# Kernel tuning notes

Measured on AMD Instinct MI355X. Metric: run time of the kernel, lower is better.

Reference implementation:

```python
import jax, jax.numpy as jnp
import numpy as np
import math

B, S, D, H = 2, 2048, 768, 12
HD = D // H


def setup_inputs() -> dict:
    key = jax.random.key(0)
    ks = jax.random.split(key, 9)
    scale = 1.0 / math.sqrt(D)
    x = jax.random.normal(ks[0], (B, S, D), dtype=jnp.float32)
    # causal mask: True where attention is allowed (query i attends to key j<=i)
    mask = jnp.tril(jnp.ones((S, S), dtype=bool))[None, None]  # [1,1,S,S]
    wq = jax.random.normal(ks[1], (D, D), dtype=jnp.float32) * scale
    bq = jnp.zeros((D,), dtype=jnp.float32)
    wk = jax.random.normal(ks[2], (D, D), dtype=jnp.float32) * scale
    bk = jnp.zeros((D,), dtype=jnp.float32)
    wv = jax.random.normal(ks[3], (D, D), dtype=jnp.float32) * scale
    bv = jnp.zeros((D,), dtype=jnp.float32)
    wo = jax.random.normal(ks[4], (D, D), dtype=jnp.float32) * scale
    bo = jnp.zeros((D,), dtype=jnp.float32)
    return {"x": x, "mask": mask, "wq": wq, "bq": bq, "wk": wk, "bk": bk,
            "wv": wv, "bv": bv, "wo": wo, "bo": bo}


def reference(x, mask, wq, bq, wk, bk, wv, bv, wo, bo):
    b, s, d = x.shape
    # projections (flax Linear: y = x @ kernel + bias)
    q = (x @ wq + bq).reshape(b, s, H, HD).transpose(0, 2, 1, 3)  # [b,h,s,hd]
    k = (x @ wk + bk).reshape(b, s, H, HD).transpose(0, 2, 1, 3)
    v = (x @ wv + bv).reshape(b, s, H, HD).transpose(0, 2, 1, 3)
    scores = jnp.einsum('bhqd,bhkd->bhqk', q, k) / math.sqrt(HD)  # [b,h,s,s]
    scores = jnp.where(mask, scores, -jnp.inf)
    attn = jax.nn.softmax(scores, axis=-1)
    out = jnp.einsum('bhqk,bhkd->bhqd', attn, v)  # [b,h,s,hd]
    out = out.transpose(0, 2, 1, 3).reshape(b, s, d)
    return out @ wo + bo
```

## Files before the change

kernel.cpp:

```cpp
#include <hip/hip_runtime.h>
#include <math.h>

#define BATCH 2
#define SEQ   2048
#define DMODEL 768
#define NHEAD 12
#define HDIM  64

typedef unsigned short u16;
typedef __attribute__((ext_vector_type(8))) short bf16x8;
typedef __attribute__((ext_vector_type(4))) float f32x4;
typedef __attribute__((ext_vector_type(8))) unsigned short us8;
typedef __attribute__((ext_vector_type(4))) unsigned short us4;

__device__ __forceinline__ u16 f2bf(float f) {
    union { float f; unsigned u; } v; v.f = f;
    unsigned u = v.u;
    u += 0x7fff + ((u >> 16) & 1);
    return (u16)(u >> 16);
}

__device__ __forceinline__ u16 f2bf_trunc(float f) {
    union { float f; unsigned u; } v; v.f = f;
    return (u16)(v.u >> 16);
}

__device__ __forceinline__ void g2l16(const void* g, void* l) {
    __builtin_amdgcn_global_load_lds(
        (const __attribute__((address_space(1))) unsigned int*)g,
        (__attribute__((address_space(3))) unsigned int*)(unsigned int)(unsigned long long)(uintptr_t)l,
        16, 0, 0);
}

__global__ __launch_bounds__(256) void prep(const float* __restrict__ x,
                                            const float* __restrict__ w0,
                                            const float* __restrict__ w1,
                                            const float* __restrict__ w2,
                                            const float* __restrict__ w3,
                                            u16* __restrict__ xb,
                                            u16* __restrict__ Wt_all) {
    __shared__ float t[32][33];
    const int bid = blockIdx.x;
    if (bid < 3072) {
        int i = bid * 256 + threadIdx.x;
        float4 v = ((const float4*)x)[i];
        us4 o;
        o.x = f2bf(v.x); o.y = f2bf(v.y); o.z = f2bf(v.z); o.w = f2bf(v.w);
        *(us4*)&xb[(size_t)i * 4] = o;
    } else {
        const int wid = bid - 3072;
        const int z  = wid / 576;
        const int rr = wid % 576;
        const int by = rr / 24, bx = rr % 24;
        const float* W = z == 0 ? w0 : z == 1 ? w1 : z == 2 ? w2 : w3;
        u16* Wt = Wt_all + (size_t)z * DMODEL * DMODEL;

        int tx = threadIdx.x & 31, ty = threadIdx.x >> 5;
        int xg = bx * 32 + tx;
        #pragma unroll
        for (int j = 0; j < 32; j += 8)
            t[ty + j][tx] = W[(size_t)(by * 32 + ty + j) * DMODEL + xg];
        __syncthreads();
        int x2 = by * 32 + tx;
        #pragma unroll
        for (int j = 0; j < 32; j += 8)
            Wt[(size_t)(bx * 32 + ty + j) * DMODEL + x2] = f2bf(t[tx][ty + j]);
    }
}

__device__ __forceinline__ void mfma_loop(const u16* __restrict__ Ag,
                                          const u16* __restrict__ Bt,
                                          int m0, int n0, int tid,
                                          u16* As, u16* Bs,
                                          f32x4 acc[4][4]) {
    const int lane = tid & 63;
    const int quad = lane >> 4, l16 = lane & 15;
    const int w    = tid >> 6;
    const int wm   = w >> 1, wn = w & 1;
    const int rowA = tid >> 2;
    const int kch  = (tid & 3) * 8;

    for (int k0 = 0; k0 < DMODEL; k0 += 32) {
        const u16* Agk = Ag + (size_t)m0 * DMODEL + k0;
        const u16* Btk = Bt + (size_t)n0 * DMODEL + k0;
        g2l16(Agk + (size_t)rowA * DMODEL + kch,        As + tid * 8);
        g2l16(Agk + (size_t)(rowA + 64) * DMODEL + kch, As + 2048 + tid * 8);
        g2l16(Btk + (size_t)rowA * DMODEL + kch,        Bs + tid * 8);
        g2l16(Btk + (size_t)(rowA + 64) * DMODEL + kch, Bs + 2048 + tid * 8);
        __syncthreads();

        bf16x8 af[4], bfr[4];
        #pragma unroll
        for (int i = 0; i < 4; ++i)
            af[i] = *(const bf16x8*)&As[(wm * 64 + i * 16 + l16) * 32 + quad * 8];
        #pragma unroll
        for (int j = 0; j < 4; ++j)
            bfr[j] = *(const bf16x8*)&Bs[(wn * 64 + j * 16 + l16) * 32 + quad * 8];
        #pragma unroll
        for (int i = 0; i < 4; ++i)
            #pragma unroll
            for (int j = 0; j < 4; ++j)
                acc[i][j] = __builtin_amdgcn_mfma_f32_16x16x32_bf16(af[i], bfr[j], acc[i][j], 0, 0, 0);
        __syncthreads();
    }
}

__global__ __launch_bounds__(256) void gemm_qkv(
    const u16* __restrict__ xb, const u16* __restrict__ WtQK,
    const u16* __restrict__ WtV,
    const float* __restrict__ bq, const float* __restrict__ bk,
    const float* __restrict__ bv,
    u16* __restrict__ QK, u16* __restrict__ Vt) {

    __shared__ __align__(16) u16 As[128 * 32];
    __shared__ __align__(16) u16 Bs[128 * 32];

    const int tid  = threadIdx.x;
    const int lane = tid & 63;
    const int w    = tid >> 6;
    const int quad = lane >> 4, l16 = lane & 15;
    const int wm   = w >> 1, wn = w & 1;
    const int bid  = blockIdx.x;

    f32x4 acc[4][4] = {};

    if (bid < 384) {
        const int m0 = (bid & 31) * 128, n0 = (bid >> 5) * 128;
        mfma_loop(xb, WtQK, m0, n0, tid, As, Bs, acc);

        const size_t n_elem = (size_t)BATCH * SEQ * DMODEL;
        #pragma unroll
        for (int j = 0; j < 4; ++j) {
            const int n     = n0 + wn * 64 + j * 16 + l16;
            const int which = n / 768;
            const int nn    = n - which * 768;
            const float bias  = (which == 0 ? bq : bk)[nn];
            const float scale = (which == 0) ? 0.125f : 1.0f;
            const int h = nn >> 6, hd = nn & 63;
            u16* outw = QK + (size_t)which * n_elem;
            #pragma unroll
            for (int i = 0; i < 4; ++i) {
                const int mbase = m0 + wm * 64 + i * 16 + quad * 4;
                #pragma unroll
                for (int r = 0; r < 4; ++r) {
                    const int m  = mbase + r;
                    const int b_ = m >> 11, s_ = m & 2047;
                    outw[(size_t)((b_ * NHEAD + h) * SEQ + s_) * HDIM + hd] =
                        f2bf((acc[i][j][r] + bias) * scale);
                }
            }
        }
    } else {
        const int vid = bid - 384;
        const int m0 = (vid % 6) * 128, n0 = (vid / 6) * 128;
        mfma_loop(WtV, xb, m0, n0, tid, As, Bs, acc);

        #pragma unroll
        for (int i = 0; i < 4; ++i) {
            const int rbase = m0 + wm * 64 + i * 16 + quad * 4;
            #pragma unroll
            for (int r = 0; r < 4; ++r) {
                const int row_g = rbase + r;
                const float bias = bv[row_g];
                const int h = row_g >> 6, hd = row_g & 63;
                #pragma unroll
                for (int j = 0; j < 4; ++j) {
                    const int col_g = n0 + wn * 64 + j * 16 + l16;
                    const int b_ = col_g >> 11, s_ = col_g & 2047;
                    Vt[(size_t)((b_ * NHEAD + h) * HDIM + hd) * SEQ + s_] =
                        f2bf(acc[i][j][r] + bias);
                }
            }
        }
    }
}

__global__ __launch_bounds__(256) void gemm_out(
    const u16* __restrict__ Ag, const u16* __restrict__ Bt,
    const float* __restrict__ bo, float* __restrict__ out) {

    __shared__ __align__(16) u16 As[64 * 32];
    __shared__ __align__(16) u16 Bs[64 * 32];

    const int tid  = threadIdx.x;
    const int lane = tid & 63;
    const int w    = tid >> 6;
    const int quad = lane >> 4, l16 = lane & 15;
    const int wm   = w >> 1, wn = w & 1;
    const int m0 = blockIdx.x * 64, n0 = blockIdx.y * 64;

    const int rowA = tid >> 2;
    const int kch  = (tid & 3) * 8;

    f32x4 acc[2][2] = {};

    for (int k0 = 0; k0 < DMODEL; k0 += 32) {
        g2l16(Ag + (size_t)(m0 + rowA) * DMODEL + k0 + kch, As + tid * 8);
        g2l16(Bt + (size_t)(n0 + rowA) * DMODEL + k0 + kch, Bs + tid * 8);
        __syncthreads();

        bf16x8 af[2], bfr[2];
        #pragma unroll
        for (int i = 0; i < 2; ++i)
            af[i] = *(const bf16x8*)&As[(wm * 32 + i * 16 + l16) * 32 + quad * 8];
        #pragma unroll
        for (int j = 0; j < 2; ++j)
            bfr[j] = *(const bf16x8*)&Bs[(wn * 32 + j * 16 + l16) * 32 + quad * 8];
        #pragma unroll
        for (int i = 0; i < 2; ++i)
            #pragma unroll
            for (int j = 0; j < 2; ++j)
                acc[i][j] = __builtin_amdgcn_mfma_f32_16x16x32_bf16(af[i], bfr[j], acc[i][j], 0, 0, 0);
        __syncthreads();
    }

    #pragma unroll
    for (int i = 0; i < 2; ++i) {
        const int mbase = m0 + wm * 32 + i * 16 + quad * 4;
        #pragma unroll
        for (int r = 0; r < 4; ++r) {
            const int m = mbase + r;
            #pragma unroll
            for (int j = 0; j < 2; ++j) {
                const int n = n0 + wn * 32 + j * 16 + l16;
                out[(size_t)m * DMODEL + n] = acc[i][j][r] + bo[n];
            }
        }
    }
}

__global__ __launch_bounds__(256) void flash_attn_mfma(
    const u16* __restrict__ Q, const u16* __restrict__ K,
    const u16* __restrict__ Vt, u16* __restrict__ A) {

    __shared__ __align__(16) u16 Kl[64 * 72];
    __shared__ __align__(16) u16 Vl[64 * 72];
    __shared__ __align__(16) u16 Pl[4][16 * 72];

    const int tid  = threadIdx.x;
    const int lane = tid & 63;
    const int w    = tid >> 6;
    const int quad = lane >> 4;
    const int l16  = lane & 15;

    const int bh = blockIdx.x;
    const int p  = blockIdx.y;
    const int uq = (w < 2) ? p : 63 - p;
    const int wrow0 = uq * 32 + (w & 1) * 16;
    const int wlast = wrow0 + 15;

    const size_t base = (size_t)bh * SEQ * HDIM;
    const u16* Qg = Q + base;
    const u16* Kg = K + base;
    const u16* Vg = Vt + base;

    bf16x8 qf0 = *(const bf16x8*)&Qg[(size_t)(wrow0 + l16) * 64 + quad * 8];
    bf16x8 qf1 = *(const bf16x8*)&Qg[(size_t)(wrow0 + l16) * 64 + quad * 8 + 32];

    f32x4 o[4] = {};
    float l_acc[4] = {0.f, 0.f, 0.f, 0.f};

    const int qrow = wrow0 + quad * 4;
    const int uB = 63 - p;
    const int tc = (32 * uB + 31) / 64 + 1;

    for (int t2 = 0; t2 < tc; ++t2) {
        const int j0 = t2 * 64;
        __syncthreads();

        #pragma unroll
        for (int r = 0; r < 2; ++r) {
            int e = tid + r * 256;
            int row = e >> 3, col = (e & 7) * 8;
            *(us8*)&Kl[row * 72 + col] = *(const us8*)&Kg[(size_t)(j0 + row) * 64 + col];
        }
        #pragma unroll
        for (int r = 0; r < 2; ++r) {
            int e = tid + r * 256;
            int d = e >> 3, kc = (e & 7) * 8;
            *(us8*)&Vl[d * 72 + kc] = *(const us8*)&Vg[(size_t)d * SEQ + j0 + kc];
        }
        __syncthreads();

        if (j0 > wlast) continue;

        f32x4 s[4];
        #pragma unroll
        for (int c4 = 0; c4 < 4; ++c4) {
            bf16x8 kf0 = *(const bf16x8*)&Kl[(c4 * 16 + l16) * 72 + quad * 8];
            bf16x8 kf1 = *(const bf16x8*)&Kl[(c4 * 16 + l16) * 72 + quad * 8 + 32];
            f32x4 a2 = {};
            a2 = __builtin_amdgcn_mfma_f32_16x16x32_bf16(qf0, kf0, a2, 0, 0, 0);
            a2 = __builtin_amdgcn_mfma_f32_16x16x32_bf16(qf1, kf1, a2, 0, 0, 0);
            s[c4] = a2;
        }

        if (j0 + 63 > wrow0) {
            #pragma unroll
            for (int c4 = 0; c4 < 4; ++c4) {
                int jg = j0 + c4 * 16 + l16;
                #pragma unroll
                for (int r = 0; r < 4; ++r)
                    if (jg > qrow + r) s[c4][r] = -INFINITY;
            }
        }

        #pragma unroll
        for (int c4 = 0; c4 < 4; ++c4)
            #pragma unroll
            for (int r = 0; r < 4; ++r)
                s[c4][r] = __expf(s[c4][r]);
        #pragma unroll
        for (int r = 0; r < 4; ++r)
            l_acc[r] += (s[0][r] + s[1][r]) + (s[2][r] + s[3][r]);

        u16* Pw = Pl[w];
        #pragma unroll
        for (int c4 = 0; c4 < 4; ++c4)
            #pragma unroll
            for (int r = 0; r < 4; ++r)
                Pw[(quad * 4 + r) * 72 + c4 * 16 + l16] = f2bf_trunc(s[c4][r]);
        bf16x8 pf0 = *(const bf16x8*)&Pw[l16 * 72 + quad * 8];
        bf16x8 pf1 = *(const bf16x8*)&Pw[l16 * 72 + quad * 8 + 32];

        #pragma unroll
        for (int c2 = 0; c2 < 4; ++c2) {
            bf16x8 vf0 = *(const bf16x8*)&Vl[(c2 * 16 + l16) * 72 + quad * 8];
            bf16x8 vf1 = *(const bf16x8*)&Vl[(c2 * 16 + l16) * 72 + quad * 8 + 32];
            o[c2] = __builtin_amdgcn_mfma_f32_16x16x32_bf16(pf0, vf0, o[c2], 0, 0, 0);
            o[c2] = __builtin_amdgcn_mfma_f32_16x16x32_bf16(pf1, vf1, o[c2], 0, 0, 0);
        }
    }

    #pragma unroll
    for (int off = 1; off < 16; off <<= 1)
        #pragma unroll
        for (int r = 0; r < 4; ++r)
            l_acc[r] += __shfl_xor(l_acc[r], off);

    const int b = bh / NHEAD, h = bh % NHEAD;
    #pragma unroll
    for (int r = 0; r < 4; ++r) {
        float inv = 1.0f / l_acc[r];
        int sg = qrow + r;
        u16* dst = A + ((size_t)(b * SEQ + sg)) * DMODEL + h * HDIM;
        #pragma unroll
        for (int c2 = 0; c2 < 4; ++c2)
            dst[c2 * 16 + l16] = f2bf(o[c2][r] * inv);
    }
}

extern "C" void kernel_launch(void* const* d_in, const int* in_sizes, int n_in,
                              void* d_out, int out_size, void* d_ws, size_t ws_size,
                              hipStream_t stream) {
    const float* x  = (const float*)d_in[0];
    const float* wq = (const float*)d_in[2];
    const float* bq = (const float*)d_in[3];
    const float* wk = (const float*)d_in[4];
    const float* bk = (const float*)d_in[5];
    const float* wv = (const float*)d_in[6];
    const float* bv = (const float*)d_in[7];
    const float* wo = (const float*)d_in[8];
    const float* bo = (const float*)d_in[9];
    float* out = (float*)d_out;

    const size_t n_elem = (size_t)BATCH * SEQ * DMODEL;
    const size_t w_elem = (size_t)DMODEL * DMODEL;

    u16* xb     = (u16*)d_ws;
    u16* Wt_all = xb + n_elem;
    u16* Qw     = Wt_all + 4 * w_elem;
    u16* Kw     = Qw + n_elem;
    u16* Vtw    = Kw + n_elem;
    u16* Aw     = Vtw + n_elem;

    dim3 blk(256);

    prep<<<dim3(3072 + 2304), blk, 0, stream>>>(x, wq, wk, wv, wo, xb, Wt_all);

    gemm_qkv<<<dim3(384 + 192), blk, 0, stream>>>(xb, Wt_all,
                                                  Wt_all + 2 * w_elem,
                                                  bq, bk, bv, Qw, Vtw);

    flash_attn_mfma<<<dim3(24, 32), blk, 0, stream>>>(Qw, Kw, Vtw, Aw);

    gemm_out<<<dim3(64, 12), blk, 0, stream>>>(Aw, Wt_all + 3 * w_elem, bo, out);
}
```

Baseline: 180.7 us.

## Fuse all four kernels into one persistent kernel with grid barriers

Replaces the four separate launches (prep, QKV GEMM, flash attention, output GEMM) with a single 768-block kernel whose stages are separated by atomic-counter grid barriers. The QKV GEMM tiles are reshaped to 128x96 and 96x128 so every block has work in each stage. The aim is to remove launch gaps and tail effects between kernels. The cost is barrier spin overhead, an extra memset launch, and the assumption that all 768 blocks are co-resident, which risks deadlock otherwise.

Result: slower. 540.9 us (+199.3%).

```diff
diff --git a/kernel.cpp b/kernel.cpp
--- a/kernel.cpp
+++ b/kernel.cpp
@@ -6,6 +6,7 @@
 #define DMODEL 768
 #define NHEAD 12
 #define HDIM  64
+#define NBLK  768
 
 typedef unsigned short u16;
 typedef __attribute__((ext_vector_type(8))) short bf16x8;
@@ -32,112 +33,124 @@
         16, 0, 0);
 }
 
-__global__ __launch_bounds__(256) void prep(const float* __restrict__ x,
-                                            const float* __restrict__ w0,
-                                            const float* __restrict__ w1,
-                                            const float* __restrict__ w2,
-                                            const float* __restrict__ w3,
-                                            u16* __restrict__ xb,
-                                            u16* __restrict__ Wt_all) {
-    __shared__ float t[32][33];
-    const int bid = blockIdx.x;
-    if (bid < 3072) {
-        int i = bid * 256 + threadIdx.x;
-        float4 v = ((const float4*)x)[i];
-        us4 o;
-        o.x = f2bf(v.x); o.y = f2bf(v.y); o.z = f2bf(v.z); o.w = f2bf(v.w);
-        *(us4*)&xb[(size_t)i * 4] = o;
-    } else {
-        const int wid = bid - 3072;
-        const int z  = wid / 576;
-        const int rr = wid % 576;
-        const int by = rr / 24, bx = rr % 24;
-        const float* W = z == 0 ? w0 : z == 1 ? w1 : z == 2 ? w2 : w3;
-        u16* Wt = Wt_all + (size_t)z * DMODEL * DMODEL;
-
-        int tx = threadIdx.x & 31, ty = threadIdx.x >> 5;
-        int xg = bx * 32 + tx;
-        #pragma unroll
-        for (int j = 0; j < 32; j += 8)
-            t[ty + j][tx] = W[(size_t)(by * 32 + ty + j) * DMODEL + xg];
-        __syncthreads();
-        int x2 = by * 32 + tx;
-        #pragma unroll
-        for (int j = 0; j < 32; j += 8)
-            Wt[(size_t)(bx * 32 + ty + j) * DMODEL + x2] = f2bf(t[tx][ty + j]);
-    }
-}
-
-__device__ __forceinline__ void mfma_loop(const u16* __restrict__ Ag,
-                                          const u16* __restrict__ Bt,
-                                          int m0, int n0, int tid,
-                                          u16* As, u16* Bs,
-                                          f32x4 acc[4][4]) {
-    const int lane = tid & 63;
-    const int quad = lane >> 4, l16 = lane & 15;
-    const int w    = tid >> 6;
-    const int wm   = w >> 1, wn = w & 1;
-    const int rowA = tid >> 2;
-    const int kch  = (tid & 3) * 8;
-
-    for (int k0 = 0; k0 < DMODEL; k0 += 32) {
-        const u16* Agk = Ag + (size_t)m0 * DMODEL + k0;
-        const u16* Btk = Bt + (size_t)n0 * DMODEL + k0;
-        g2l16(Agk + (size_t)rowA * DMODEL + kch,        As + tid * 8);
-        g2l16(Agk + (size_t)(rowA + 64) * DMODEL + kch, As + 2048 + tid * 8);
-        g2l16(Btk + (size_t)rowA * DMODEL + kch,        Bs + tid * 8);
-        g2l16(Btk + (size_t)(rowA + 64) * DMODEL + kch, Bs + 2048 + tid * 8);
-        __syncthreads();
-
-        bf16x8 af[4], bfr[4];
-        #pragma unroll
-        for (int i = 0; i < 4; ++i)
-            af[i] = *(const bf16x8*)&As[(wm * 64 + i * 16 + l16) * 32 + quad * 8];
-        #pragma unroll
-        for (int j = 0; j < 4; ++j)
-            bfr[j] = *(const bf16x8*)&Bs[(wn * 64 + j * 16 + l16) * 32 + quad * 8];
-        #pragma unroll
-        for (int i = 0; i < 4; ++i)
-            #pragma unroll
-            for (int j = 0; j < 4; ++j)
-                acc[i][j] = __builtin_amdgcn_mfma_f32_16x16x32_bf16(af[i], bfr[j], acc[i][j], 0, 0, 0);
-        __syncthreads();
-    }
-}
-
-__global__ __launch_bounds__(256) void gemm_qkv(
-    const u16* __restrict__ xb, const u16* __restrict__ WtQK,
-    const u16* __restrict__ WtV,
+__device__ __forceinline__ void grid_barrier(unsigned* cnt, unsigned target) {
+    __syncthreads();
+    if (threadIdx.x == 0) {
+        __threadfence();
+        atomicAdd(cnt, 1u);
+        while (__hip_atomic_load(cnt, __ATOMIC_RELAXED,
+                                 __HIP_MEMORY_SCOPE_AGENT) < target)
+            __builtin_amdgcn_s_sleep(8);
+        __threadfence();
+    }
+    __syncthreads();
+}
+
+__device__ __forceinline__ void stage_rows(const u16* g, u16* lds, int nrows,
+                                           int tid) {
+    const int row = tid >> 2, col = (tid & 3) * 8;
+    g2l16(g + (size_t)row * DMODEL + col, lds + tid * 8);
+    if (nrows == 128) {
+        g2l16(g + (size_t)(row + 64) * DMODEL + col, lds + 2048 + tid * 8);
+    } else if (nrows == 96) {
+        if (tid < 128)
+            g2l16(g + (size_t)(row + 64) * DMODEL + col, lds + 2048 + tid * 8);
+    }
+}
+
+__global__ __launch_bounds__(256, 4) void fused(
+    const float* __restrict__ x,
+    const float* __restrict__ w0, const float* __restrict__ w1,
+    const float* __restrict__ w2, const float* __restrict__ w3,
     const float* __restrict__ bq, const float* __restrict__ bk,
-    const float* __restrict__ bv,
-    u16* __restrict__ QK, u16* __restrict__ Vt) {
-
-    __shared__ __align__(16) u16 As[128 * 32];
-    __shared__ __align__(16) u16 Bs[128 * 32];
-
+    const float* __restrict__ bv, const float* __restrict__ bo,
+    u16* xb, u16* Wt_all, u16* Qw, u16* Vtw, u16* Aw,
+    float* out, unsigned* cnt) {
+
+    __shared__ union {
+        struct { u16 A[128 * 32]; u16 B[128 * 32]; } g;
+        struct { u16 Kl[64 * 72]; u16 Vl[64 * 72];
+                 u16 Pl[4][16 * 72]; } f;
+        float t[32][33];
+    } sm;
+
+    const int b    = blockIdx.x;
     const int tid  = threadIdx.x;
     const int lane = tid & 63;
     const int w    = tid >> 6;
     const int quad = lane >> 4, l16 = lane & 15;
     const int wm   = w >> 1, wn = w & 1;
-    const int bid  = blockIdx.x;
-
-    f32x4 acc[4][4] = {};
-
-    if (bid < 384) {
-        const int m0 = (bid & 31) * 128, n0 = (bid >> 5) * 128;
-        mfma_loop(xb, WtQK, m0, n0, tid, As, Bs, acc);
-
-        const size_t n_elem = (size_t)BATCH * SEQ * DMODEL;
-        #pragma unroll
-        for (int j = 0; j < 4; ++j) {
-            const int n     = n0 + wn * 64 + j * 16 + l16;
+
+    const size_t n_elem = (size_t)BATCH * SEQ * DMODEL;
+    const size_t w_elem = (size_t)DMODEL * DMODEL;
+    const u16* WtQK = Wt_all;
+    const u16* WtV  = Wt_all + 2 * w_elem;
+    const u16* WtO  = Wt_all + 3 * w_elem;
+    u16* Kw = Qw + n_elem;
+
+    #pragma unroll 1
+    for (int ui = 0; ui < 7; ++ui) {
+        const int u = b * 7 + ui;
+        if (u < 3072) {
+            int i = u * 256 + tid;
+            float4 v = ((const float4*)x)[i];
+            us4 o;
+            o.x = f2bf(v.x); o.y = f2bf(v.y); o.z = f2bf(v.z); o.w = f2bf(v.w);
+            *(us4*)&xb[(size_t)i * 4] = o;
+        } else {
+            const int wid = u - 3072;
+            const int z  = wid / 576;
+            const int rr = wid % 576;
+            const int by = rr / 24, bx = rr % 24;
+            const float* W = z == 0 ? w0 : z == 1 ? w1 : z == 2 ? w2 : w3;
+            u16* Wt = Wt_all + (size_t)z * w_elem;
+            int tx = tid & 31, ty = tid >> 5;
+            int xg = bx * 32 + tx;
+            #pragma unroll
+            for (int j = 0; j < 32; j += 8)
+                sm.t[ty + j][tx] = W[(size_t)(by * 32 + ty + j) * DMODEL + xg];
+            __syncthreads();
+            int x2 = by * 32 + tx;
+            #pragma unroll
+            for (int j = 0; j < 32; j += 8)
+                Wt[(size_t)(bx * 32 + ty + j) * DMODEL + x2] = f2bf(sm.t[tx][ty + j]);
+            __syncthreads();
+        }
+    }
+
+    grid_barrier(cnt, NBLK);
+
+    if (b < 512) {
+        const int m0 = (b >> 4) * 128;
+        const int n0 = (b & 15) * 96;
+        f32x4 acc[4][3] = {};
+        for (int k0 = 0; k0 < DMODEL; k0 += 32) {
+            stage_rows(xb  + (size_t)m0 * DMODEL + k0, sm.g.A, 128, tid);
+            stage_rows(WtQK + (size_t)n0 * DMODEL + k0, sm.g.B,  96, tid);
+            __syncthreads();
+            bf16x8 af[4], bfr[3];
+            #pragma unroll
+            for (int i = 0; i < 4; ++i)
+                af[i] = *(const bf16x8*)&sm.g.A[(wm * 64 + i * 16 + l16) * 32 + quad * 8];
+            #pragma unroll
+            for (int j = 0; j < 3; ++j)
+                bfr[j] = *(const bf16x8*)&sm.g.B[(wn * 48 + j * 16 + l16) * 32 + quad * 8];
+            #pragma unroll
+            for (int i = 0; i < 4; ++i)
+                #pragma unroll
+                for (int j = 0; j < 3; ++j)
+                    acc[i][j] = __builtin_amdgcn_mfma_f32_16x16x32_bf16(af[i], bfr[j], acc[i][j], 0, 0, 0);
+            __syncthreads();
+        }
+        #pragma unroll
+        for (int j = 0; j < 3; ++j) {
+            const int n     = n0 + wn * 48 + j * 16 + l16;
             const int which = n / 768;
             const int nn    = n - which * 768;
             const float bias  = (which == 0 ? bq : bk)[nn];
             const float scale = (which == 0) ? 0.125f : 1.0f;
             const int h = nn >> 6, hd = nn & 63;
-            u16* outw = QK + (size_t)which * n_elem;
+            u16* outw = Qw + (size_t)which * n_elem;
             #pragma unroll
             for (int i = 0; i < 4; ++i) {
                 const int mbase = m0 + wm * 64 + i * 16 + quad * 4;
@@ -151,13 +164,31 @@
             }
         }
     } else {
-        const int vid = bid - 384;
-        const int m0 = (vid % 6) * 128, n0 = (vid / 6) * 128;
-        mfma_loop(WtV, xb, m0, n0, tid, As, Bs, acc);
-
-        #pragma unroll
-        for (int i = 0; i < 4; ++i) {
-            const int rbase = m0 + wm * 64 + i * 16 + quad * 4;
+        const int vj = b - 512;
+        const int m0 = (vj & 7) * 96;
+        const int n0 = (vj >> 3) * 128;
+        f32x4 acc[3][4] = {};
+        for (int k0 = 0; k0 < DMODEL; k0 += 32) {
+            stage_rows(WtV + (size_t)m0 * DMODEL + k0, sm.g.A,  96, tid);
+            stage_rows(xb  + (size_t)n0 * DMODEL + k0, sm.g.B, 128, tid);
+            __syncthreads();
+            bf16x8 af[3], bfr[4];
+            #pragma unroll
+            for (int i = 0; i < 3; ++i)
+                af[i] = *(const bf16x8*)&sm.g.A[(wm * 48 + i * 16 + l16) * 32 + quad * 8];
+            #pragma unroll
+            for (int j = 0; j < 4; ++j)
+                bfr[j] = *(const bf16x8*)&sm.g.B[(wn * 64 + j * 16 + l16) * 32 + quad * 8];
+            #pragma unroll
+            for (int i = 0; i < 3; ++i)
+                #pragma unroll
+                for (int j = 0; j < 4; ++j)
+                    acc[i][j] = __builtin_amdgcn_mfma_f32_16x16x32_bf16(af[i], bfr[j], acc[i][j], 0, 0, 0);
+            __syncthreads();
+        }
+        #pragma unroll
+        for (int i = 0; i < 3; ++i) {
+            const int rbase = m0 + wm * 48 + i * 16 + quad * 4;
             #pragma unroll
             for (int r = 0; r < 4; ++r) {
                 const int row_g = rbase + r;
@@ -167,186 +198,161 @@
                 for (int j = 0; j < 4; ++j) {
                     const int col_g = n0 + wn * 64 + j * 16 + l16;
                     const int b_ = col_g >> 11, s_ = col_g & 2047;
-                    Vt[(size_t)((b_ * NHEAD + h) * HDIM + hd) * SEQ + s_] =
+                    Vtw[(size_t)((b_ * NHEAD + h) * HDIM + hd) * SEQ + s_] =
                         f2bf(acc[i][j][r] + bias);
                 }
             }
         }
     }
-}
-
-__global__ __launch_bounds__(256) void gemm_out(
-    const u16* __restrict__ Ag, const u16* __restrict__ Bt,
-    const float* __restrict__ bo, float* __restrict__ out) {
-
-    __shared__ __align__(16) u16 As[64 * 32];
-    __shared__ __align__(16) u16 Bs[64 * 32];
-
-    const int tid  = threadIdx.x;
-    const int lane = tid & 63;
-    const int w    = tid >> 6;
-    const int quad = lane >> 4, l16 = lane & 15;
-    const int wm   = w >> 1, wn = w & 1;
-    const int m0 = blockIdx.x * 64, n0 = blockIdx.y * 64;
-
-    const int rowA = tid >> 2;
-    const int kch  = (tid & 3) * 8;
-
-    f32x4 acc[2][2] = {};
-
-    for (int k0 = 0; k0 < DMODEL; k0 += 32) {
-        g2l16(Ag + (size_t)(m0 + rowA) * DMODEL + k0 + kch, As + tid * 8);
-        g2l16(Bt + (size_t)(n0 + rowA) * DMODEL + k0 + kch, Bs + tid * 8);
-        __syncthreads();
-
-        bf16x8 af[2], bfr[2];
-        #pragma unroll
-        for (int i = 0; i < 2; ++i)
-            af[i] = *(const bf16x8*)&As[(wm * 32 + i * 16 + l16) * 32 + quad * 8];
-        #pragma unroll
-        for (int j = 0; j < 2; ++j)
-            bfr[j] = *(const bf16x8*)&Bs[(wn * 32 + j * 16 + l16) * 32 + quad * 8];
-        #pragma unroll
-        for (int i = 0; i < 2; ++i)
+
+    grid_barrier(cnt, 2 * NBLK);
+
+    {
+        const int bh = b % 24;
+        const int p  = b / 24;
+        const int uq = (w < 2) ? p : 63 - p;
+        const int wrow0 = uq * 32 + (w & 1) * 16;
+        const int wlast = wrow0 + 15;
+
+        const size_t base = (size_t)bh * SEQ * HDIM;
+        const u16* Qg = Qw + base;
+        const u16* Kg = Kw + base;
+        const u16* Vg = Vtw + base;
+
+        bf16x8 qf0 = *(const bf16x8*)&Qg[(size_t)(wrow0 + l16) * 64 + quad * 8];
+        bf16x8 qf1 = *(const bf16x8*)&Qg[(size_t)(wrow0 + l16) * 64 + quad * 8 + 32];
+
+        f32x4 o[4] = {};
+        float l_acc[4] = {0.f, 0.f, 0.f, 0.f};
+
+        const int qrow = wrow0 + quad * 4;
+        const int uB = 63 - p;
+        const int tc = (32 * uB + 31) / 64 + 1;
+
+        for (int t2 = 0; t2 < tc; ++t2) {
+            const int j0 = t2 * 64;
+            __syncthreads();
+            #pragma unroll
+            for (int r = 0; r < 2; ++r) {
+                int e = tid + r * 256;
+                int row = e >> 3, col = (e & 7) * 8;
+                *(us8*)&sm.f.Kl[row * 72 + col] =
+                    *(const us8*)&Kg[(size_t)(j0 + row) * 64 + col];
+            }
+            #pragma unroll
+            for (int r = 0; r < 2; ++r) {
+                int e = tid + r * 256;
+                int d = e >> 3, kc = (e & 7) * 8;
+                *(us8*)&sm.f.Vl[d * 72 + kc] =
+                    *(const us8*)&Vg[(size_t)d * SEQ + j0 + kc];
+            }
+            __syncthreads();
+
+            if (j0 > wlast) continue;
+
+            f32x4 s[4];
+            #pragma unroll
+            for (int c4 = 0; c4 < 4; ++c4) {
+                bf16x8 kf0 = *(const bf16x8*)&sm.f.Kl[(c4 * 16 + l16) * 72 + quad * 8];
+                bf16x8 kf1 = *(const bf16x8*)&sm.f.Kl[(c4 * 16 + l16) * 72 + quad * 8 + 32];
+                f32x4 a2 = {};
+                a2 = __builtin_amdgcn_mfma_f32_16x16x32_bf16(qf0, kf0, a2, 0, 0, 0);
+                a2 = __builtin_amdgcn_mfma_f32_16x16x32_bf16(qf1, kf1, a2, 0, 0, 0);
+                s[c4] = a2;
+            }
+
+            if (j0 + 63 > wrow0) {
+                #pragma unroll
+                for (int c4 = 0; c4 < 4; ++c4) {
+                    int jg = j0 + c4 * 16 + l16;
+                    #pragma unroll
+                    for (int r = 0; r < 4; ++r)
+                        if (jg > qrow + r) s[c4][r] = -INFINITY;
+                }
+            }
+
+            #pragma unroll
+            for (int c4 = 0; c4 < 4; ++c4)
+                #pragma unroll
+                for (int r = 0; r < 4; ++r)
+                    s[c4][r] = __expf(s[c4][r]);
+            #pragma unroll
+            for (int r = 0; r < 4; ++r)
+                l_acc[r] += (s[0][r] + s[1][r]) + (s[2][r] + s[3][r]);
+
+            u16* Pw = sm.f.Pl[w];
+            #pragma unroll
+            for (int c4 = 0; c4 < 4; ++c4)
+                #pragma unroll
+                for (int r = 0; r < 4; ++r)
+                    Pw[(quad * 4 + r) * 72 + c4 * 16 + l16] = f2bf_trunc(s[c4][r]);
+            bf16x8 pf0 = *(const bf16x8*)&Pw[l16 * 72 + quad * 8];
+            bf16x8 pf1 = *(const bf16x8*)&Pw[l16 * 72 + quad * 8 + 32];
+
+            #pragma unroll
+            for (int c2 = 0; c2 < 4; ++c2) {
+                bf16x8 vf0 = *(const bf16x8*)&sm.f.Vl[(c2 * 16 + l16) * 72 + quad * 8];
+                bf16x8 vf1 = *(const bf16x8*)&sm.f.Vl[(c2 * 16 + l16) * 72 + quad * 8 + 32];
+                o[c2] = __builtin_amdgcn_mfma_f32_16x16x32_bf16(pf0, vf0, o[c2], 0, 0, 0);
+                o[c2] = __builtin_amdgcn_mfma_f32_16x16x32_bf16(pf1, vf1, o[c2], 0, 0, 0);
+            }
+        }
+
+        #pragma unroll
+        for (int off = 1; off < 16; off <<= 1)
+            #pragma unroll
+            for (int r = 0; r < 4; ++r)
+                l_acc[r] += __shfl_xor(l_acc[r], off);
+
+        const int bb = bh / NHEAD, h = bh % NHEAD;
+        #pragma unroll
+        for (int r = 0; r < 4; ++r) {
+            float inv = 1.0f / l_acc[r];
+            int sg = qrow + r;
+            u16* dst = Aw + ((size_t)(bb * SEQ + sg)) * DMODEL + h * HDIM;
+            #pragma unroll
+            for (int c2 = 0; c2 < 4; ++c2)
+                dst[c2 * 16 + l16] = f2bf(o[c2][r] * inv);
+        }
+    }
+
+    grid_barrier(cnt, 3 * NBLK);
+
+    {
+        const int m0 = (b & 63) * 64;
+        const int n0 = (b >> 6) * 64;
+        f32x4 acc[2][2] = {};
+        for (int k0 = 0; k0 < DMODEL; k0 += 32) {
+            stage_rows(Aw  + (size_t)m0 * DMODEL + k0, sm.g.A, 64, tid);
+            stage_rows(WtO + (size_t)n0 * DMODEL + k0, sm.g.B, 64, tid);
+            __syncthreads();
+            bf16x8 af[2], bfr[2];
+            #pragma unroll
+            for (int i = 0; i < 2; ++i)
+                af[i] = *(const bf16x8*)&sm.g.A[(wm * 32 + i * 16 + l16) * 32 + quad * 8];
             #pragma unroll
             for (int j = 0; j < 2; ++j)
-                acc[i][j] = __builtin_amdgcn_mfma_f32_16x16x32_bf16(af[i], bfr[j], acc[i][j], 0, 0, 0);
-        __syncthreads();
-    }
-
-    #pragma unroll
-    for (int i = 0; i < 2; ++i) {
-        const int mbase = m0 + wm * 32 + i * 16 + quad * 4;
-        #pragma unroll
-        for (int r = 0; r < 4; ++r) {
-            const int m = mbase + r;
-            #pragma unroll
-            for (int j = 0; j < 2; ++j) {
-                const int n = n0 + wn * 32 + j * 16 + l16;
-                out[(size_t)m * DMODEL + n] = acc[i][j][r] + bo[n];
-            }
-        }
-    }
-}
-
-__global__ __launch_bounds__(256) void flash_attn_mfma(
-    const u16* __restrict__ Q, const u16* __restrict__ K,
-    const u16* __restrict__ Vt, u16* __restrict__ A) {
-
-    __shared__ __align__(16) u16 Kl[64 * 72];
-    __shared__ __align__(16) u16 Vl[64 * 72];
-    __shared__ __align__(16) u16 Pl[4][16 * 72];
-
-    const int tid  = threadIdx.x;
-    const int lane = tid & 63;
-    const int w    = tid >> 6;
-    const int quad = lane >> 4;
-    const int l16  = lane & 15;
-
-    const int bh = blockIdx.x;
-    const int p  = blockIdx.y;
-    const int uq = (w < 2) ? p : 63 - p;
-    const int wrow0 = uq * 32 + (w & 1) * 16;
-    const int wlast = wrow0 + 15;
-
-    const size_t base = (size_t)bh * SEQ * HDIM;
-    const u16* Qg = Q + base;
-    const u16* Kg = K + base;
-    const u16* Vg = Vt + base;
-
-    bf16x8 qf0 = *(const bf16x8*)&Qg[(size_t)(wrow0 + l16) * 64 + quad * 8];
-    bf16x8 qf1 = *(const bf16x8*)&Qg[(size_t)(wrow0 + l16) * 64 + quad * 8 + 32];
-
-    f32x4 o[4] = {};
-    float l_acc[4] = {0.f, 0.f, 0.f, 0.f};
-
-    const int qrow = wrow0 + quad * 4;
-    const int uB = 63 - p;
-    const int tc = (32 * uB + 31) / 64 + 1;
-
-    for (int t2 = 0; t2 < tc; ++t2) {
-        const int j0 = t2 * 64;
-        __syncthreads();
-
-        #pragma unroll
-        for (int r = 0; r < 2; ++r) {
-            int e = tid + r * 256;
-            int row = e >> 3, col = (e & 7) * 8;
-            *(us8*)&Kl[row * 72 + col] = *(const us8*)&Kg[(size_t)(j0 + row) * 64 + col];
-        }
-        #pragma unroll
-        for (int r = 0; r < 2; ++r) {
-            int e = tid + r * 256;
-            int d = e >> 3, kc = (e & 7) * 8;
-            *(us8*)&Vl[d * 72 + kc] = *(const us8*)&Vg[(size_t)d * SEQ + j0 + kc];
-        }
-        __syncthreads();
-
-        if (j0 > wlast) continue;
-
-        f32x4 s[4];
-        #pragma unroll
-        for (int c4 = 0; c4 < 4; ++c4) {
-            bf16x8 kf0 = *(const bf16x8*)&Kl[(c4 * 16 + l16) * 72 + quad * 8];
-            bf16x8 kf1 = *(const bf16x8*)&Kl[(c4 * 16 + l16) * 72 + quad * 8 + 32];
-            f32x4 a2 = {};
-            a2 = __builtin_amdgcn_mfma_f32_16x16x32_bf16(qf0, kf0, a2, 0, 0, 0);
-            a2 = __builtin_amdgcn_mfma_f32_16x16x32_bf16(qf1, kf1, a2, 0, 0, 0);
-            s[c4] = a2;
-        }
-
-        if (j0 + 63 > wrow0) {
-            #pragma unroll
-            for (int c4 = 0; c4 < 4; ++c4) {
-                int jg = j0 + c4 * 16 + l16;
-                #pragma unroll
-                for (int r = 0; r < 4; ++r)
-                    if (jg > qrow + r) s[c4][r] = -INFINITY;
-            }
-        }
-
-        #pragma unroll
-        for (int c4 = 0; c4 < 4; ++c4)
-            #pragma unroll
-            for (int r = 0; r < 4; ++r)
-                s[c4][r] = __expf(s[c4][r]);
-        #pragma unroll
-        for (int r = 0; r < 4; ++r)
-            l_acc[r] += (s[0][r] + s[1][r]) + (s[2][r] + s[3][r]);
-
-        u16* Pw = Pl[w];
-        #pragma unroll
-        for (int c4 = 0; c4 < 4; ++c4)
-            #pragma unroll
-            for (int r = 0; r < 4; ++r)
-                Pw[(quad * 4 + r) * 72 + c4 * 16 + l16] = f2bf_trunc(s[c4][r]);
-        bf16x8 pf0 = *(const bf16x8*)&Pw[l16 * 72 + quad * 8];
-        bf16x8 pf1 = *(const bf16x8*)&Pw[l16 * 72 + quad * 8 + 32];
-
-        #pragma unroll
-        for (int c2 = 0; c2 < 4; ++c2) {
-            bf16x8 vf0 = *(const bf16x8*)&Vl[(c2 * 16 + l16) * 72 + quad * 8];
-            bf16x8 vf1 = *(const bf16x8*)&Vl[(c2 * 16 + l16) * 72 + quad * 8 + 32];
-            o[c2] = __builtin_amdgcn_mfma_f32_16x16x32_bf16(pf0, vf0, o[c2], 0, 0, 0);
-            o[c2] = __builtin_amdgcn_mfma_f32_16x16x32_bf16(pf1, vf1, o[c2], 0, 0, 0);
-        }
-    }
-
-    #pragma unroll
-    for (int off = 1; off < 16; off <<= 1)
-        #pragma unroll
-        for (int r = 0; r < 4; ++r)
-            l_acc[r] += __shfl_xor(l_acc[r], off);
-
-    const int b = bh / NHEAD, h = bh % NHEAD;
-    #pragma unroll
-    for (int r = 0; r < 4; ++r) {
-        float inv = 1.0f / l_acc[r];
-        int sg = qrow + r;
-        u16* dst = A + ((size_t)(b * SEQ + sg)) * DMODEL + h * HDIM;
-        #pragma unroll
-        for (int c2 = 0; c2 < 4; ++c2)
-            dst[c2 * 16 + l16] = f2bf(o[c2][r] * inv);
+                bfr[j] = *(const bf16x8*)&sm.g.B[(wn * 32 + j * 16 + l16) * 32 + quad * 8];
+            #pragma unroll
+            for (int i = 0; i < 2; ++i)
+                #pragma unroll
+                for (int j = 0; j < 2; ++j)
+                    acc[i][j] = __builtin_amdgcn_mfma_f32_16x16x32_bf16(af[i], bfr[j], acc[i][j], 0, 0, 0);
+            __syncthreads();
+        }
+        #pragma unroll
+        for (int i = 0; i < 2; ++i) {
+            const int mbase = m0 + wm * 32 + i * 16 + quad * 4;
+            #pragma unroll
+            for (int r = 0; r < 4; ++r) {
+                const int m = mbase + r;
+                #pragma unroll
+                for (int j = 0; j < 2; ++j) {
+                    const int n = n0 + wn * 32 + j * 16 + l16;
+                    out[(size_t)m * DMODEL + n] = acc[i][j][r] + bo[n];
+                }
+            }
+        }
     }
 }
 
@@ -370,19 +376,14 @@
     u16* xb     = (u16*)d_ws;
     u16* Wt_all = xb + n_elem;
     u16* Qw     = Wt_all + 4 * w_elem;
-    u16* Kw     = Qw + n_elem;
-    u16* Vtw    = Kw + n_elem;
+    u16* Vtw    = Qw + 2 * n_elem;
     u16* Aw     = Vtw + n_elem;
 
-    dim3 blk(256);
-
-    prep<<<dim3(3072 + 2304), blk, 0, stream>>>(x, wq, wk, wv, wo, xb, Wt_all);
-
-    gemm_qkv<<<dim3(384 + 192), blk, 0, stream>>>(xb, Wt_all,
-                                                  Wt_all + 2 * w_elem,
-                                                  bq, bk, bv, Qw, Vtw);
-
-    flash_attn_mfma<<<dim3(24, 32), blk, 0, stream>>>(Qw, Kw, Vtw, Aw);
-
-    gemm_out<<<dim3(64, 12), blk, 0, stream>>>(Aw, Wt_all + 3 * w_elem, bo, out);
-}
+    size_t cnt_off = (ws_size - 256) & ~(size_t)63;
+    unsigned* cnt = (unsigned*)((char*)d_ws + cnt_off);
+    hipMemsetAsync(cnt, 0, 256, stream);
+
+    fused<<<dim3(NBLK), dim3(256), 0, stream>>>(
+        x, wq, wk, wv, wo, bq, bk, bv, bo,
+        xb, Wt_all, Qw, Vtw, Aw, out, cnt);
+}
```
